# Kernel optimization log

Measured on AMD Instinct MI355X. Metric: run time of the kernel, lower is better.

Reference implementation:

```python
import jax, jax.numpy as jnp
import numpy as np
from math import factorial, sqrt

# static config matching cg_interaction(l1=3, l2=3, l_middel=2, l_out=3, channel=128)
L1 = 3; L2 = 3; MIDDLE = 2; LOUT = 3; CHANNEL = 128; EDGES = 65536
DIM1 = (L1 + 1) ** 2  # 16
DIM2 = (L2 + 1) ** 2  # 16


def _su2_cg(j1, m1, j2, m2, j3, m3):
    # standard Clebsch-Gordan coefficient <j1 m1 j2 m2 | j3 m3> (Racah formula)
    if m3 != m1 + m2:
        return 0.0
    f = factorial
    pref = sqrt((2 * j3 + 1) * f(j3 + j1 - j2) * f(j3 - j1 + j2) * f(j1 + j2 - j3) / f(j1 + j2 + j3 + 1))
    pref *= sqrt(f(j3 + m3) * f(j3 - m3) * f(j1 - m1) * f(j1 + m1) * f(j2 - m2) * f(j2 + m2))
    kmin = max(0, j2 - j3 - m1, j1 - j3 + m2)
    kmax = min(j1 + j2 - j3, j1 - m1, j2 + m2)
    s = 0.0
    for k in range(kmin, kmax + 1):
        s += (-1) ** k / (f(k) * f(j1 + j2 - j3 - k) * f(j1 - m1 - k) * f(j2 + m2 - k) * f(j3 - j2 + m1 + k) * f(j3 - j1 - m2 + k))
    return pref * s


def _q_real_to_complex(l):
    # e3nn change-of-basis real->complex spherical harmonics
    q = np.zeros((2 * l + 1, 2 * l + 1), dtype=np.complex128)
    for m in range(-l, 0):
        q[l + m, l + abs(m)] = 1 / sqrt(2)
        q[l + m, l - abs(m)] = -1j / sqrt(2)
    q[l, l] = 1.0
    for m in range(1, l + 1):
        q[l + m, l + abs(m)] = (-1) ** m / sqrt(2)
        q[l + m, l - abs(m)] = 1j * (-1) ** m / sqrt(2)
    return (-1j) ** l * q


def _w3j(l1, l2, l3):
    # real Wigner-3j tensor, unit Frobenius norm (e3nn convention up to global sign)
    C = np.zeros((2 * l1 + 1, 2 * l2 + 1, 2 * l3 + 1))
    for m1 in range(-l1, l1 + 1):
        for m2 in range(-l2, l2 + 1):
            m3 = m1 + m2
            if abs(m3) <= l3:
                C[l1 + m1, l2 + m2, l3 + m3] = _su2_cg(l1, m1, l2, m2, l3, m3)
    Q1, Q2, Q3 = _q_real_to_complex(l1), _q_real_to_complex(l2), _q_real_to_complex(l3)
    Cr = np.einsum('ij,kl,nm,ikm->jln', Q1, Q2, np.conj(Q3), C.astype(np.complex128))
    Cr = np.real(Cr)
    return (Cr / np.linalg.norm(Cr)).astype(np.float32)


# output irrep entries (mul, l): [scalars(0e), gate-scalars(0e), gated l=1.., ...]
ENTRIES_CG = [(CHANNEL, 0), (CHANNEL * MIDDLE, 0)] + [(CHANNEL, l) for l in range(1, MIDDLE + 1)]
ENTRIES_ALL = [(1, 0), (LOUT, 0)] + [(1, l) for l in range(1, LOUT + 1)]


def _paths(entries):
    p = []
    for ei, (mul, lo) in enumerate(entries):
        for la in range(L1 + 1):
            for lb in range(L2 + 1):
                if (la + lb + lo) % 2 == 0 and abs(la - lb) <= lo <= la + lb:
                    p.append((la, lb, ei))
    return p


PATHS_CG = _paths(ENTRIES_CG)
PATHS_ALL = _paths(ENTRIES_ALL)
NW_CG = sum(ENTRIES_CG[ei][0] for _, _, ei in PATHS_CG)   # 3200
NW_ALL = sum(ENTRIES_ALL[ei][0] for _, _, ei in PATHS_ALL)  # 35
NB_CG = sum(m for m, l in ENTRIES_CG if l == 0)  # 384
NB_ALL = sum(m for m, l in ENTRIES_ALL if l == 0)  # 4

_keys = set()
for la, lb, ei in PATHS_CG:
    _keys.add((la, lb, ENTRIES_CG[ei][1]))
for la, lb, ei in PATHS_ALL:
    _keys.add((la, lb, ENTRIES_ALL[ei][1]))
W3J = {k: jnp.asarray(_w3j(*k)) for k in sorted(_keys)}


def _tp(x, y, w, b, entries, paths):
    # fully-connected tensor product (mul-1 inputs) with per-output-entry
    # sqrt((2l+1)/num_paths) normalization and bias on 0e entries
    blocks = [None] * len(entries)
    npaths = [0] * len(entries)
    for _, _, ei in paths:
        npaths[ei] += 1
    off = 0
    for la, lb, ei in paths:
        mul, lo = entries[ei]
        xs = x[:, la * la:(la + 1) * (la + 1)]
        ys = y[:, lb * lb:(lb + 1) * (lb + 1)]
        z = jnp.einsum('ei,ej,ijk->ek', xs, ys, W3J[(la, lb, lo)])  # (E, 2lo+1)
        c = z[:, None, :] * w[off:off + mul][None, :, None]         # (E, mul, 2lo+1)
        blocks[ei] = c if blocks[ei] is None else blocks[ei] + c
        off += mul
    boff = 0
    outs = []
    for ei, (mul, lo) in enumerate(entries):
        blk = blocks[ei] * np.float32(sqrt((2 * lo + 1) / max(npaths[ei], 1)))
        if lo == 0:
            blk = blk + b[boff:boff + mul][None, :, None]
            boff += mul
        outs.append(blk)
    return outs


def _forward(x, y, w_cg, b_cg, w_all, b_all):
    # --- cg branch: channelled mid-degree TP + SwishGate + degree reshape ---
    outs = _tp(x, y, w_cg, b_cg, ENTRIES_CG, PATHS_CG)
    sc = jax.nn.silu(outs[0][..., 0])                    # (E, C)
    gates = jax.nn.sigmoid(outs[1][..., 0])              # (E, C*MIDDLE)
    rows = [sc[:, None, :]]                              # degree-0 row of reshape output
    for l in range(1, MIDDLE + 1):
        g = gates[:, (l - 1) * CHANNEL:l * CHANNEL]      # (E, C)
        gated = outs[1 + l] * g[:, :, None]              # (E, C, 2l+1)
        rows.append(jnp.transpose(gated, (0, 2, 1)))     # (E, 2l+1, C)
    cg_low = jnp.concatenate(rows, axis=1)               # (E, (MIDDLE+1)^2, C)
    # --- cg_all branch: mul-1 TP up to l_out + SwishGate ---
    outs_a = _tp(x, y, w_all, b_all, ENTRIES_ALL, PATHS_ALL)
    pieces = [jax.nn.silu(outs_a[0][..., 0])]            # (E, 1)
    ga = jax.nn.sigmoid(outs_a[1][..., 0])               # (E, LOUT)
    for l in range(1, LOUT + 1):
        pieces.append(outs_a[1 + l][:, 0, :] * ga[:, l - 1:l])  # (E, 2l+1)
    cg_all = jnp.concatenate(pieces, axis=1)             # (E, (LOUT+1)^2)
    return cg_low, cg_all


def setup_inputs() -> dict:
    key = jax.random.key(0)
    k1, k2, k3, k4, k5, k6 = jax.random.split(key, 6)
    x = jax.random.normal(k1, (EDGES, DIM1), jnp.float32)
    y = jax.random.normal(k2, (EDGES, DIM2), jnp.float32)
    w_cg = jax.random.normal(k3, (NW_CG,), jnp.float32) * 0.3
    b_cg = jax.random.normal(k4, (NB_CG,), jnp.float32) * 0.1
    w_all = jax.random.normal(k5, (NW_ALL,), jnp.float32) * 0.3
    b_all = jax.random.normal(k6, (NB_ALL,), jnp.float32) * 0.1
    return {"x": x, "y": y, "w_cg": w_cg, "b_cg": b_cg, "w_all": w_all, "b_all": b_all}


def reference(x, y, w_cg, b_cg, w_all, b_all):
    return _forward(x, y, w_cg, b_cg, w_all, b_all)
```

## Files before the change

kernel.cpp:

```cpp
#include <hip/hip_runtime.h>
#include <utility>

namespace w3j_gen {

struct FactT { double f[16]; };
constexpr FactT make_fact() {
    FactT t{}; t.f[0] = 1.0;
    for (int i = 1; i < 16; i++) t.f[i] = t.f[i-1] * (double)i;
    return t;
}
constexpr FactT FT = make_fact();

constexpr double csqrt(double x) {
    if (x <= 0.0) return 0.0;
    double g = x < 1.0 ? 1.0 : x;
    for (int i = 0; i < 80; i++) g = 0.5 * (g + x / g);
    return g;
}

constexpr int imax3(int a, int b, int c) { int m = a; if (b > m) m = b; if (c > m) m = c; return m; }
constexpr int imin3(int a, int b, int c) { int m = a; if (b < m) m = b; if (c < m) m = c; return m; }

constexpr double su2_cg(int j1, int m1, int j2, int m2, int j3, int m3) {
    if (m3 != m1 + m2) return 0.0;
    double pref = csqrt((double)(2*j3+1) * FT.f[j3+j1-j2] * FT.f[j3-j1+j2] * FT.f[j1+j2-j3] / FT.f[j1+j2+j3+1]);
    pref *= csqrt(FT.f[j3+m3] * FT.f[j3-m3] * FT.f[j1-m1] * FT.f[j1+m1] * FT.f[j2-m2] * FT.f[j2+m2]);
    int kmin = imax3(0, j2-j3-m1, j1-j3+m2);
    int kmax = imin3(j1+j2-j3, j1-m1, j2+m2);
    double s = 0.0;
    for (int k = kmin; k <= kmax; k++) {
        double d = FT.f[k] * FT.f[j1+j2-j3-k] * FT.f[j1-m1-k] * FT.f[j2+m2-k] * FT.f[j3-j2+m1+k] * FT.f[j3-j1-m2+k];
        s += ((k & 1) ? -1.0 : 1.0) / d;
    }
    return pref * s;
}

struct CD { double re, im; };
struct QT { CD q[7][7]; };

constexpr QT make_q(int l) {
    QT t{};
    const double is2 = csqrt(0.5);
    for (int m = -l; m < 0; m++) {
        t.q[l+m][l-m].re = is2;
        t.q[l+m][l+m].im = -is2;
    }
    t.q[l][l].re = 1.0;
    for (int m = 1; m <= l; m++) {
        double s = (m & 1) ? -1.0 : 1.0;
        t.q[l+m][l+m].re = s * is2;
        t.q[l+m][l-m].im = s * is2;
    }
    CD ph = {1.0, 0.0};
    if (l % 4 == 1) ph = {0.0, -1.0};
    else if (l % 4 == 2) ph = {-1.0, 0.0};
    else if (l % 4 == 3) ph = {0.0, 1.0};
    for (int i = 0; i < 7; i++)
        for (int j = 0; j < 7; j++) {
            CD a = t.q[i][j];
            t.q[i][j] = { ph.re*a.re - ph.im*a.im, ph.re*a.im + ph.im*a.re };
        }
    return t;
}

struct Tab { float v[245]; };

constexpr Tab make_w3j(int l1, int l2, int l3) {
    const int n1 = 2*l1+1, n2 = 2*l2+1, n3 = 2*l3+1;
    double C[7][7][7] = {};
    for (int m1 = -l1; m1 <= l1; m1++)
        for (int m2 = -l2; m2 <= l2; m2++) {
            int m3 = m1 + m2;
            if (m3 >= -l3 && m3 <= l3)
                C[l1+m1][l2+m2][l3+m3] = su2_cg(l1, m1, l2, m2, l3, m3);
        }
    QT Q1 = make_q(l1), Q2 = make_q(l2), Q3 = make_q(l3);
    CD T1[7][7][7] = {};
    for (int j = 0; j < n1; j++)
        for (int k = 0; k < n2; k++)
            for (int m = 0; m < n3; m++) {
                double sr = 0, si = 0;
                for (int i = 0; i < n1; i++) {
                    double cv = C[i][k][m];
                    sr += Q1.q[i][j].re * cv;
                    si += Q1.q[i][j].im * cv;
                }
                T1[j][k][m] = {sr, si};
            }
    CD T2[7][7][7] = {};
    for (int j = 0; j < n1; j++)
        for (int l = 0; l < n2; l++)
            for (int m = 0; m < n3; m++) {
                double sr = 0, si = 0;
                for (int k = 0; k < n2; k++) {
                    CD a = Q2.q[k][l], b = T1[j][k][m];
                    sr += a.re*b.re - a.im*b.im;
                    si += a.re*b.im + a.im*b.re;
                }
                T2[j][l][m] = {sr, si};
            }
    double Cr[7][7][7] = {};
    double nrm2 = 0.0;
    for (int j = 0; j < n1; j++)
        for (int l = 0; l < n2; l++)
            for (int n = 0; n < n3; n++) {
                double s = 0;
                for (int m = 0; m < n3; m++) {
                    CD a = Q3.q[n][m], b = T2[j][l][m];
                    s += a.re*b.re + a.im*b.im;
                }
                Cr[j][l][n] = s;
                nrm2 += s * s;
            }
    double inv = 1.0 / csqrt(nrm2);
    Tab t{};
    for (int j = 0; j < n1; j++)
        for (int l = 0; l < n2; l++)
            for (int n = 0; n < n3; n++)
                t.v[(j*n2 + l)*n3 + n] = (float)(Cr[j][l][n] * inv);
    return t;
}

constexpr Tab T0  = make_w3j(0,0,0);
constexpr Tab T1_ = make_w3j(1,1,0);
constexpr Tab T2_ = make_w3j(2,2,0);
constexpr Tab T3_ = make_w3j(3,3,0);
constexpr Tab T4  = make_w3j(0,1,1);
constexpr Tab T5  = make_w3j(1,0,1);
constexpr Tab T6  = make_w3j(1,2,1);
constexpr Tab T7  = make_w3j(2,1,1);
constexpr Tab T8  = make_w3j(2,3,1);
constexpr Tab T9  = make_w3j(3,2,1);
constexpr Tab T10 = make_w3j(0,2,2);
constexpr Tab T11 = make_w3j(1,1,2);
constexpr Tab T12 = make_w3j(1,3,2);
constexpr Tab T13 = make_w3j(2,0,2);
constexpr Tab T14 = make_w3j(2,2,2);
constexpr Tab T15 = make_w3j(3,1,2);
constexpr Tab T16 = make_w3j(3,3,2);
constexpr Tab T17 = make_w3j(0,3,3);
constexpr Tab T18 = make_w3j(1,2,3);
constexpr Tab T19 = make_w3j(2,1,3);
constexpr Tab T20 = make_w3j(2,3,3);
constexpr Tab T21 = make_w3j(3,0,3);
constexpr Tab T22 = make_w3j(3,2,3);

constexpr int KLA[23]   = {0,1,2,3, 0,1,1,2,2,3, 0,1,1,2,2,3,3, 0,1,2,2,3,3};
constexpr int KLB[23]   = {0,1,2,3, 1,0,2,1,3,2, 2,1,3,0,2,1,3, 3,2,1,3,0,2};
constexpr int KLO[23]   = {0,0,0,0, 1,1,1,1,1,1, 2,2,2,2,2,2,2, 3,3,3,3,3,3};
constexpr int KZOFF[23] = {0,1,2,3, 4,7,10,13,16,19, 22,27,32,37,42,47,52, 57,64,71,78,85,92};

struct Term { int i, j, k; float w; };
struct TermList { Term t[1875]; int koff[24]; int n; };

constexpr TermList build_terms() {
    TermList L{};
    const Tab* ts[23] = {&T0,&T1_,&T2_,&T3_,&T4,&T5,&T6,&T7,&T8,&T9,&T10,&T11,
                         &T12,&T13,&T14,&T15,&T16,&T17,&T18,&T19,&T20,&T21,&T22};
    for (int key = 0; key < 23; key++) {
        L.koff[key] = L.n;
        const int la = KLA[key], lb = KLB[key], lo = KLO[key];
        const int n1 = 2*la+1, n2 = 2*lb+1, n3 = 2*lo+1;
        for (int i = 0; i < n1; i++)
            for (int j = 0; j < n2; j++)
                for (int k = 0; k < n3; k++) {
                    float w = ts[key]->v[(i*n2+j)*n3+k];
                    float aw = w < 0 ? -w : w;
                    if (aw > 1e-6f) {
                        L.t[L.n].i = la*la + i;
                        L.t[L.n].j = lb*lb + j;
                        L.t[L.n].k = KZOFF[key] + k;
                        L.t[L.n].w = w;
                        L.n++;
                    }
                }
    }
    L.koff[23] = L.n;
    return L;
}
constexpr TermList TL = build_terms();

}

template <int KEY, size_t... I>
__device__ __forceinline__ void term_unroll(float* __restrict__ acc,
                                            const float* __restrict__ xv,
                                            const float* __restrict__ yv,
                                            std::index_sequence<I...>) {
    constexpr int t0 = w3j_gen::TL.koff[KEY];
    ((acc[w3j_gen::TL.t[t0 + I].k - w3j_gen::KZOFF[KEY]] +=
          w3j_gen::TL.t[t0 + I].w * xv[w3j_gen::TL.t[t0 + I].i] * yv[w3j_gen::TL.t[t0 + I].j]), ...);
}

template <int KEY>
__device__ __forceinline__ void key_accum(float* __restrict__ zrow,
                                          const float* __restrict__ xv,
                                          const float* __restrict__ yv) {
    constexpr int n3 = 2 * w3j_gen::KLO[KEY] + 1;
    constexpr int nt = w3j_gen::TL.koff[KEY + 1] - w3j_gen::TL.koff[KEY];
    float acc[n3] = {};
    term_unroll<KEY>(acc, xv, yv, std::make_index_sequence<(size_t)nt>{});
    #pragma unroll
    for (int k = 0; k < n3; k++) zrow[w3j_gen::KZOFF[KEY] + k] = acc[k];
}

template <size_t... K>
__device__ __forceinline__ void all_keys(float* __restrict__ zrow,
                                         const float* __restrict__ xv,
                                         const float* __restrict__ yv,
                                         std::index_sequence<K...>) {
    (key_accum<(int)K>(zrow, xv, yv), ...);
}

#define N_EDGES   65536
#define TILE      64
#define ZROW      108
#define ALL_BASE  75497472ull

__device__ __forceinline__ float sigmoidf_(float v) { return 1.0f / (1.0f + __expf(-v)); }

__global__ __launch_bounds__(256)
void cg_interaction_kernel(
    const float* __restrict__ x, const float* __restrict__ y,
    const float* __restrict__ w_cg, const float* __restrict__ b_cg,
    const float* __restrict__ w_all, const float* __restrict__ b_all,
    float* __restrict__ out)
{
    __shared__ __align__(16) float zs[TILE][ZROW];

    const int tid = threadIdx.x;
    const int e0 = blockIdx.x * TILE;

    if (tid < TILE) {
        const int e = e0 + tid;
        float xv[16], yv[16];
        const float4* xp = (const float4*)(x + (size_t)e * 16);
        const float4* yp = (const float4*)(y + (size_t)e * 16);
        #pragma unroll
        for (int q = 0; q < 4; q++) {
            float4 v = xp[q];
            xv[4*q+0] = v.x; xv[4*q+1] = v.y; xv[4*q+2] = v.z; xv[4*q+3] = v.w;
            float4 u = yp[q];
            yv[4*q+0] = u.x; yv[4*q+1] = u.y; yv[4*q+2] = u.z; yv[4*q+3] = u.w;
        }
        all_keys(&zs[tid][0], xv, yv, std::make_index_sequence<23>{});
    }
    __syncthreads();

    const int half = tid >> 7;
    const int c = tid & 127;

    float wc0[4], wc1[4], wc2[4];
    #pragma unroll
    for (int p = 0; p < 4; p++) {
        wc0[p] = w_cg[p * 128 + c];
        wc1[p] = w_cg[512 + p * 256 + c];
        wc2[p] = w_cg[640 + p * 256 + c];
    }
    float wl1[6];
    #pragma unroll
    for (int p = 0; p < 6; p++) wl1[p] = w_cg[1536 + p * 128 + c];
    float wl2[7];
    #pragma unroll
    for (int p = 0; p < 7; p++) wl2[p] = w_cg[2304 + p * 128 + c];
    const float b0 = b_cg[c], b1 = b_cg[128 + c], b2 = b_cg[256 + c];

    const float SQ12 = 0.70710678118654752f;
    const float SQ57 = 0.84515425472851657f;
    const float SQ76 = 1.08012344973464f;

    float gw0 = 0.f, gw1 = 0.f, gw2 = 0.f, gw3 = 0.f, gb = 0.f, ascale = 0.f;
    int zbase = 4, zstride = 3;
    float aw[7] = {0.f,0.f,0.f,0.f,0.f,0.f,0.f};
    if (c == 0) {
        gw0 = w_all[0]; gw1 = w_all[1]; gw2 = w_all[2]; gw3 = w_all[3]; gb = b_all[0];
    } else if (c < 4) {
        gw0 = w_all[4]; gw1 = w_all[7]; gw2 = w_all[10]; gw3 = w_all[13]; gb = b_all[1];
        ascale = SQ12; zbase = 4 + (c - 1); zstride = 3;
        #pragma unroll
        for (int p = 0; p < 6; p++) aw[p] = w_all[16 + p];
    } else if (c < 9) {
        gw0 = w_all[5]; gw1 = w_all[8]; gw2 = w_all[11]; gw3 = w_all[14]; gb = b_all[2];
        ascale = SQ57; zbase = 22 + (c - 4); zstride = 5;
        #pragma unroll
        for (int p = 0; p < 7; p++) aw[p] = w_all[22 + p];
    } else if (c < 16) {
        gw0 = w_all[6]; gw1 = w_all[9]; gw2 = w_all[12]; gw3 = w_all[15]; gb = b_all[3];
        ascale = SQ76; zbase = 57 + (c - 9); zstride = 7;
        #pragma unroll
        for (int p = 0; p < 6; p++) aw[p] = w_all[29 + p];
    }

    for (int t = half; t < TILE; t += 2) {
        const size_t e = (size_t)(e0 + t);
        const float* zrow = &zs[t][0];

        float zz[60];
        #pragma unroll
        for (int q = 0; q < 15; q++) {
            float4 v = *(const float4*)(zrow + 4 * q);
            zz[4*q+0] = v.x; zz[4*q+1] = v.y; zz[4*q+2] = v.z; zz[4*q+3] = v.w;
        }

        float u0 = (zz[0]*wc0[0] + zz[1]*wc0[1] + zz[2]*wc0[2] + zz[3]*wc0[3]) * 0.5f + b0;
        float u1 = (zz[0]*wc1[0] + zz[1]*wc1[1] + zz[2]*wc1[2] + zz[3]*wc1[3]) * 0.5f + b1;
        float u2 = (zz[0]*wc2[0] + zz[1]*wc2[1] + zz[2]*wc2[2] + zz[3]*wc2[3]) * 0.5f + b2;
        float sc = u0 * sigmoidf_(u0);
        float g1 = sigmoidf_(u1) * SQ12;
        float g2 = sigmoidf_(u2) * SQ57;

        float* o = out + e * 1152 + c;
        __builtin_nontemporal_store(sc, o);
        #pragma unroll
        for (int k = 0; k < 3; k++) {
            float s = 0.0f;
            #pragma unroll
            for (int p = 0; p < 6; p++) s += zz[4 + 3*p + k] * wl1[p];
            __builtin_nontemporal_store(s * g1, o + (1 + k) * 128);
        }
        #pragma unroll
        for (int k = 0; k < 5; k++) {
            float s = 0.0f;
            #pragma unroll
            for (int p = 0; p < 7; p++) s += zz[22 + 5*p + k] * wl2[p];
            __builtin_nontemporal_store(s * g2, o + (4 + k) * 128);
        }

        if (c < 16) {
            float g = (zz[0]*gw0 + zz[1]*gw1 + zz[2]*gw2 + zz[3]*gw3) * 0.5f + gb;
            float v;
            if (c == 0) {
                v = g * sigmoidf_(g);
            } else {
                float s = 0.0f;
                #pragma unroll
                for (int p = 0; p < 7; p++) {
                    float zv = zrow[zbase + zstride * p];
                    s += aw[p] * zv;
                }
                v = s * ascale * sigmoidf_(g);
            }
            __builtin_nontemporal_store(v, out + ALL_BASE + e * 16 + c);
        }
    }
}

extern "C" void kernel_launch(void* const* d_in, const int* in_sizes, int n_in,
                              void* d_out, int out_size, void* d_ws, size_t ws_size,
                              hipStream_t stream) {
    const float* x     = (const float*)d_in[0];
    const float* y     = (const float*)d_in[1];
    const float* w_cg  = (const float*)d_in[2];
    const float* b_cg  = (const float*)d_in[3];
    const float* w_all = (const float*)d_in[4];
    const float* b_all = (const float*)d_in[5];
    float* out = (float*)d_out;

    dim3 grid(N_EDGES / TILE), block(256);
    hipLaunchKernelGGL(cg_interaction_kernel, grid, block, 0, stream,
                       x, y, w_cg, b_cg, w_all, b_all, out);
}
```

Baseline: 345.5 us.

## Split CG term computation across all threads and vectorize channel outputs

The Wigner-3j product stage now spreads its keys over four thread groups, so all 256 threads work instead of only 64. The channel stage gives each thread four channels with float4 weight loads and 128-bit nontemporal stores, and walks edges with eight thread groups. The per-edge l_out branch moves out of the main loop into a separate pass run by 128 threads, which removes divergence in the hot loop. Launch bounds now request 2 blocks per CU, which adds register pressure because each thread holds four times as many weights.

New measurement: 333.4 us. 1.04x faster.

```diff
diff --git a/kernel.cpp b/kernel.cpp
--- a/kernel.cpp
+++ b/kernel.cpp
@@ -180,6 +180,14 @@
 }
 constexpr TermList TL = build_terms();
 
+constexpr int find_split(int target) {
+    for (int k = 0; k <= 23; k++) if (TL.koff[k] >= target) return k;
+    return 23;
+}
+constexpr int S1 = find_split(TL.n / 4);
+constexpr int S2 = find_split(TL.n / 2);
+constexpr int S3 = find_split(3 * TL.n / 4);
+
 }
 
 template <int KEY, size_t... I>
@@ -204,12 +212,12 @@
     for (int k = 0; k < n3; k++) zrow[w3j_gen::KZOFF[KEY] + k] = acc[k];
 }
 
-template <size_t... K>
-__device__ __forceinline__ void all_keys(float* __restrict__ zrow,
-                                         const float* __restrict__ xv,
-                                         const float* __restrict__ yv,
-                                         std::index_sequence<K...>) {
-    (key_accum<(int)K>(zrow, xv, yv), ...);
+template <int FROM, size_t... K>
+__device__ __forceinline__ void keys_range(float* __restrict__ zrow,
+                                           const float* __restrict__ xv,
+                                           const float* __restrict__ yv,
+                                           std::index_sequence<K...>) {
+    (key_accum<FROM + (int)K>(zrow, xv, yv), ...);
 }
 
 #define N_EDGES   65536
@@ -217,9 +225,11 @@
 #define ZROW      108
 #define ALL_BASE  75497472ull
 
+typedef float f32x4 __attribute__((ext_vector_type(4)));
+
 __device__ __forceinline__ float sigmoidf_(float v) { return 1.0f / (1.0f + __expf(-v)); }
 
-__global__ __launch_bounds__(256)
+__global__ __launch_bounds__(256, 2)
 void cg_interaction_kernel(
     const float* __restrict__ x, const float* __restrict__ y,
     const float* __restrict__ w_cg, const float* __restrict__ b_cg,
@@ -231,11 +241,12 @@
     const int tid = threadIdx.x;
     const int e0 = blockIdx.x * TILE;
 
-    if (tid < TILE) {
-        const int e = e0 + tid;
+    {
+        const int eidx = tid & 63;
+        const int esub = tid >> 6;
         float xv[16], yv[16];
-        const float4* xp = (const float4*)(x + (size_t)e * 16);
-        const float4* yp = (const float4*)(y + (size_t)e * 16);
+        const float4* xp = (const float4*)(x + (size_t)(e0 + eidx) * 16);
+        const float4* yp = (const float4*)(y + (size_t)(e0 + eidx) * 16);
         #pragma unroll
         for (int q = 0; q < 4; q++) {
             float4 v = xp[q];
@@ -243,58 +254,56 @@
             float4 u = yp[q];
             yv[4*q+0] = u.x; yv[4*q+1] = u.y; yv[4*q+2] = u.z; yv[4*q+3] = u.w;
         }
-        all_keys(&zs[tid][0], xv, yv, std::make_index_sequence<23>{});
+        using namespace w3j_gen;
+        float* zrow = &zs[eidx][0];
+        if (esub == 0)      keys_range<0 >(zrow, xv, yv, std::make_index_sequence<S1>{});
+        else if (esub == 1) keys_range<S1>(zrow, xv, yv, std::make_index_sequence<S2 - S1>{});
+        else if (esub == 2) keys_range<S2>(zrow, xv, yv, std::make_index_sequence<S3 - S2>{});
+        else                keys_range<S3>(zrow, xv, yv, std::make_index_sequence<23 - S3>{});
     }
     __syncthreads();
 
-    const int half = tid >> 7;
-    const int c = tid & 127;
-
-    float wc0[4], wc1[4], wc2[4];
+    const int cq = (tid & 31) << 2;
+    const int es = tid >> 5;
+
+    float w00[4][4], wg1[4][4], wg2[4][4];
     #pragma unroll
     for (int p = 0; p < 4; p++) {
-        wc0[p] = w_cg[p * 128 + c];
-        wc1[p] = w_cg[512 + p * 256 + c];
-        wc2[p] = w_cg[640 + p * 256 + c];
-    }
-    float wl1[6];
+        float4 a = *(const float4*)(w_cg + p * 128 + cq);
+        w00[p][0]=a.x; w00[p][1]=a.y; w00[p][2]=a.z; w00[p][3]=a.w;
+        float4 b = *(const float4*)(w_cg + 512 + p * 256 + cq);
+        wg1[p][0]=b.x; wg1[p][1]=b.y; wg1[p][2]=b.z; wg1[p][3]=b.w;
+        float4 d = *(const float4*)(w_cg + 640 + p * 256 + cq);
+        wg2[p][0]=d.x; wg2[p][1]=d.y; wg2[p][2]=d.z; wg2[p][3]=d.w;
+    }
+    float wl1[6][4];
     #pragma unroll
-    for (int p = 0; p < 6; p++) wl1[p] = w_cg[1536 + p * 128 + c];
-    float wl2[7];
+    for (int p = 0; p < 6; p++) {
+        float4 a = *(const float4*)(w_cg + 1536 + p * 128 + cq);
+        wl1[p][0]=a.x; wl1[p][1]=a.y; wl1[p][2]=a.z; wl1[p][3]=a.w;
+    }
+    float wl2[7][4];
     #pragma unroll
-    for (int p = 0; p < 7; p++) wl2[p] = w_cg[2304 + p * 128 + c];
-    const float b0 = b_cg[c], b1 = b_cg[128 + c], b2 = b_cg[256 + c];
+    for (int p = 0; p < 7; p++) {
+        float4 a = *(const float4*)(w_cg + 2304 + p * 128 + cq);
+        wl2[p][0]=a.x; wl2[p][1]=a.y; wl2[p][2]=a.z; wl2[p][3]=a.w;
+    }
+    float b0[4], b1[4], b2[4];
+    {
+        float4 a = *(const float4*)(b_cg + cq);
+        b0[0]=a.x; b0[1]=a.y; b0[2]=a.z; b0[3]=a.w;
+        float4 b = *(const float4*)(b_cg + 128 + cq);
+        b1[0]=b.x; b1[1]=b.y; b1[2]=b.z; b1[3]=b.w;
+        float4 d = *(const float4*)(b_cg + 256 + cq);
+        b2[0]=d.x; b2[1]=d.y; b2[2]=d.z; b2[3]=d.w;
+    }
 
     const float SQ12 = 0.70710678118654752f;
     const float SQ57 = 0.84515425472851657f;
-    const float SQ76 = 1.08012344973464f;
-
-    float gw0 = 0.f, gw1 = 0.f, gw2 = 0.f, gw3 = 0.f, gb = 0.f, ascale = 0.f;
-    int zbase = 4, zstride = 3;
-    float aw[7] = {0.f,0.f,0.f,0.f,0.f,0.f,0.f};
-    if (c == 0) {
-        gw0 = w_all[0]; gw1 = w_all[1]; gw2 = w_all[2]; gw3 = w_all[3]; gb = b_all[0];
-    } else if (c < 4) {
-        gw0 = w_all[4]; gw1 = w_all[7]; gw2 = w_all[10]; gw3 = w_all[13]; gb = b_all[1];
-        ascale = SQ12; zbase = 4 + (c - 1); zstride = 3;
-        #pragma unroll
-        for (int p = 0; p < 6; p++) aw[p] = w_all[16 + p];
-    } else if (c < 9) {
-        gw0 = w_all[5]; gw1 = w_all[8]; gw2 = w_all[11]; gw3 = w_all[14]; gb = b_all[2];
-        ascale = SQ57; zbase = 22 + (c - 4); zstride = 5;
-        #pragma unroll
-        for (int p = 0; p < 7; p++) aw[p] = w_all[22 + p];
-    } else if (c < 16) {
-        gw0 = w_all[6]; gw1 = w_all[9]; gw2 = w_all[12]; gw3 = w_all[15]; gb = b_all[3];
-        ascale = SQ76; zbase = 57 + (c - 9); zstride = 7;
-        #pragma unroll
-        for (int p = 0; p < 6; p++) aw[p] = w_all[29 + p];
-    }
-
-    for (int t = half; t < TILE; t += 2) {
-        const size_t e = (size_t)(e0 + t);
+
+    float* o = out + (size_t)(e0 + es) * 1152 + cq;
+    for (int t = es; t < TILE; t += 8, o += 8 * 1152) {
         const float* zrow = &zs[t][0];
-
         float zz[60];
         #pragma unroll
         for (int q = 0; q < 15; q++) {
@@ -302,45 +311,104 @@
             zz[4*q+0] = v.x; zz[4*q+1] = v.y; zz[4*q+2] = v.z; zz[4*q+3] = v.w;
         }
 
-        float u0 = (zz[0]*wc0[0] + zz[1]*wc0[1] + zz[2]*wc0[2] + zz[3]*wc0[3]) * 0.5f + b0;
-        float u1 = (zz[0]*wc1[0] + zz[1]*wc1[1] + zz[2]*wc1[2] + zz[3]*wc1[3]) * 0.5f + b1;
-        float u2 = (zz[0]*wc2[0] + zz[1]*wc2[1] + zz[2]*wc2[2] + zz[3]*wc2[3]) * 0.5f + b2;
-        float sc = u0 * sigmoidf_(u0);
-        float g1 = sigmoidf_(u1) * SQ12;
-        float g2 = sigmoidf_(u2) * SQ57;
-
-        float* o = out + e * 1152 + c;
-        __builtin_nontemporal_store(sc, o);
+        float sc[4], g1[4], g2[4];
+        #pragma unroll
+        for (int j = 0; j < 4; j++) {
+            float u0 = (zz[0]*w00[0][j] + zz[1]*w00[1][j] + zz[2]*w00[2][j] + zz[3]*w00[3][j]) * 0.5f + b0[j];
+            float u1 = (zz[0]*wg1[0][j] + zz[1]*wg1[1][j] + zz[2]*wg1[2][j] + zz[3]*wg1[3][j]) * 0.5f + b1[j];
+            float u2 = (zz[0]*wg2[0][j] + zz[1]*wg2[1][j] + zz[2]*wg2[2][j] + zz[3]*wg2[3][j]) * 0.5f + b2[j];
+            sc[j] = u0 * sigmoidf_(u0);
+            g1[j] = sigmoidf_(u1) * SQ12;
+            g2[j] = sigmoidf_(u2) * SQ57;
+        }
+
+        f32x4 r0 = { sc[0], sc[1], sc[2], sc[3] };
+        __builtin_nontemporal_store(r0, (f32x4*)o);
         #pragma unroll
         for (int k = 0; k < 3; k++) {
-            float s = 0.0f;
+            float s[4];
             #pragma unroll
-            for (int p = 0; p < 6; p++) s += zz[4 + 3*p + k] * wl1[p];
-            __builtin_nontemporal_store(s * g1, o + (1 + k) * 128);
+            for (int j = 0; j < 4; j++) {
+                float a = 0.0f;
+                #pragma unroll
+                for (int p = 0; p < 6; p++) a += zz[4 + 3*p + k] * wl1[p][j];
+                s[j] = a * g1[j];
+            }
+            f32x4 r = { s[0], s[1], s[2], s[3] };
+            __builtin_nontemporal_store(r, (f32x4*)(o + (1 + k) * 128));
         }
         #pragma unroll
         for (int k = 0; k < 5; k++) {
-            float s = 0.0f;
+            float s[4];
             #pragma unroll
-            for (int p = 0; p < 7; p++) s += zz[22 + 5*p + k] * wl2[p];
-            __builtin_nontemporal_store(s * g2, o + (4 + k) * 128);
-        }
-
-        if (c < 16) {
-            float g = (zz[0]*gw0 + zz[1]*gw1 + zz[2]*gw2 + zz[3]*gw3) * 0.5f + gb;
-            float v;
-            if (c == 0) {
-                v = g * sigmoidf_(g);
-            } else {
+            for (int j = 0; j < 4; j++) {
+                float a = 0.0f;
+                #pragma unroll
+                for (int p = 0; p < 7; p++) a += zz[22 + 5*p + k] * wl2[p][j];
+                s[j] = a * g2[j];
+            }
+            f32x4 r = { s[0], s[1], s[2], s[3] };
+            __builtin_nontemporal_store(r, (f32x4*)(o + (4 + k) * 128));
+        }
+    }
+
+    if (tid < 128) {
+        const int c = tid & 15;
+        const int es2 = tid >> 4;
+        const float SQ76 = 1.08012344973464f;
+
+        if (c == 0) {
+            const float gw0 = w_all[0], gw1 = w_all[1], gw2 = w_all[2], gw3 = w_all[3], gb = b_all[0];
+            for (int t = es2; t < TILE; t += 8) {
+                const float* zr = &zs[t][0];
+                float g = (zr[0]*gw0 + zr[1]*gw1 + zr[2]*gw2 + zr[3]*gw3) * 0.5f + gb;
+                __builtin_nontemporal_store(g * sigmoidf_(g), out + ALL_BASE + (size_t)(e0 + t) * 16);
+            }
+        } else if (c < 4) {
+            const float gw0 = w_all[4], gw1 = w_all[7], gw2 = w_all[10], gw3 = w_all[13], gb = b_all[1];
+            float aw[6];
+            #pragma unroll
+            for (int p = 0; p < 6; p++) aw[p] = w_all[16 + p];
+            const int zb = 4 + (c - 1);
+            for (int t = es2; t < TILE; t += 8) {
+                const float* zr = &zs[t][0];
+                float g = (zr[0]*gw0 + zr[1]*gw1 + zr[2]*gw2 + zr[3]*gw3) * 0.5f + gb;
                 float s = 0.0f;
                 #pragma unroll
-                for (int p = 0; p < 7; p++) {
-                    float zv = zrow[zbase + zstride * p];
-                    s += aw[p] * zv;
-                }
-                v = s * ascale * sigmoidf_(g);
-            }
-            __builtin_nontemporal_store(v, out + ALL_BASE + e * 16 + c);
+                for (int p = 0; p < 6; p++) s += aw[p] * zr[zb + 3*p];
+                __builtin_nontemporal_store(s * SQ12 * sigmoidf_(g),
+                                            out + ALL_BASE + (size_t)(e0 + t) * 16 + c);
+            }
+        } else if (c < 9) {
+            const float gw0 = w_all[5], gw1 = w_all[8], gw2 = w_all[11], gw3 = w_all[14], gb = b_all[2];
+            float aw[7];
+            #pragma unroll
+            for (int p = 0; p < 7; p++) aw[p] = w_all[22 + p];
+            const int zb = 22 + (c - 4);
+            for (int t = es2; t < TILE; t += 8) {
+                const float* zr = &zs[t][0];
+                float g = (zr[0]*gw0 + zr[1]*gw1 + zr[2]*gw2 + zr[3]*gw3) * 0.5f + gb;
+                float s = 0.0f;
+                #pragma unroll
+                for (int p = 0; p < 7; p++) s += aw[p] * zr[zb + 5*p];
+                __builtin_nontemporal_store(s * SQ57 * sigmoidf_(g),
+                                            out + ALL_BASE + (size_t)(e0 + t) * 16 + c);
+            }
+        } else {
+            const float gw0 = w_all[6], gw1 = w_all[9], gw2 = w_all[12], gw3 = w_all[15], gb = b_all[3];
+            float aw[6];
+            #pragma unroll
+            for (int p = 0; p < 6; p++) aw[p] = w_all[29 + p];
+            const int zb = 57 + (c - 9);
+            for (int t = es2; t < TILE; t += 8) {
+                const float* zr = &zs[t][0];
+                float g = (zr[0]*gw0 + zr[1]*gw1 + zr[2]*gw2 + zr[3]*gw3) * 0.5f + gb;
+                float s = 0.0f;
+                #pragma unroll
+                for (int p = 0; p < 6; p++) s += aw[p] * zr[zb + 7*p];
+                __builtin_nontemporal_store(s * SQ76 * sigmoidf_(g),
+                                            out + ALL_BASE + (size_t)(e0 + t) * 16 + c);
+            }
         }
     }
 }
```
